# Optimization experiments

Hardware: AMD Instinct MI355X
Metric: run time of the kernel (lower is better)

The kernel has to match this reference:

```python
import jax, jax.numpy as jnp
import numpy as np

EPS = 1e-8  # torch CosineSimilarity eps


def _l2_normalize(x):
    n = jnp.sqrt(jnp.sum(x * x, axis=-1, keepdims=True))
    return x / jnp.maximum(n, EPS)


def setup_inputs() -> dict:
    key = jax.random.key(0)
    k1, k2, k3 = jax.random.split(key, 3)
    B, D, K = 4096, 1024, 256
    datapoints = jax.random.normal(k1, (B, D), dtype=jnp.float32)
    centroid = jax.random.normal(k2, (K, D), dtype=jnp.float32)
    batch_cos_sim = jax.random.normal(k3, (B, B), dtype=jnp.float32)
    return {"datapoints": datapoints, "centroid": centroid, "batch_cos_sim": batch_cos_sim}


def reference(datapoints, centroid, batch_cos_sim):
    # --- _clustering: cosine similarity datapoints[B,D] vs centroid[K,D] (temp=1) ---
    dn = _l2_normalize(datapoints)                       # [B, D]
    cn = _l2_normalize(centroid)                         # [K, D]
    intra_cos_sim = jnp.einsum('bd,kd->bk', dn, cn)      # [B, K]
    dp_index = jnp.argmax(intra_cos_sim, axis=-1)        # [B]

    # --- _intra_class_adjacency: one-hot matmul, zero diagonal ---
    onehot = jax.nn.one_hot(dp_index, centroid.shape[0], dtype=jnp.float32)  # [B, K]
    dp_cluster = jnp.einsum('bk,ck->bc', onehot, onehot)                      # [B, B]
    B = datapoints.shape[0]
    dp_cluster = dp_cluster * (1.0 - jnp.eye(B, dtype=dp_cluster.dtype))
    index_dp = onehot.T.astype(jnp.int32)                # [K, B]

    # --- gather centroid each datapoint belongs to ---
    dp_centroid = centroid[dp_index]                     # [B, D]

    # --- provide_hard_negative: top-2, take 2nd-best centroid ---
    top_vals, top_idx = jax.lax.top_k(intra_cos_sim, 2)  # [B, 2]
    hard_neg_index = top_idx[:, 1]                       # [B]
    hard_negative = centroid[hard_neg_index]             # [B, D]

    return (intra_cos_sim, dp_index, dp_cluster, index_dp, dp_centroid,
            hard_negative, hard_neg_index, top_vals[:, 1])
```

## Files before the change

### kernel.cpp

```cpp
#include <hip/hip_runtime.h>
#include <hip/hip_bf16.h>
#include <math.h>

#define B_N 4096
#define D_N 1024
#define K_N 256
#define NSTEP 32

typedef __attribute__((ext_vector_type(8))) short bf16x8;
typedef __attribute__((ext_vector_type(8))) unsigned short u16x8;
typedef __attribute__((ext_vector_type(4))) float f32x4;

static constexpr float K_EPS = 1e-8f;

static __device__ __forceinline__ unsigned short f32_to_bf16_rne(float f) {
    unsigned x = __builtin_bit_cast(unsigned, f);
    unsigned r = (x + 0x7FFFu + ((x >> 16) & 1u)) >> 16;
    return (unsigned short)r;
}
static __device__ __forceinline__ float bf16_bits_to_f32(unsigned short h) {
    unsigned x = ((unsigned)h) << 16;
    return __builtin_bit_cast(float, x);
}
static __device__ __forceinline__ void cvt8(
    float e0, float e1, float e2, float e3,
    float e4, float e5, float e6, float e7, u16x8& hv, u16x8& lv)
{
    ushort h0=f32_to_bf16_rne(e0), h1=f32_to_bf16_rne(e1),
           h2=f32_to_bf16_rne(e2), h3=f32_to_bf16_rne(e3),
           h4=f32_to_bf16_rne(e4), h5=f32_to_bf16_rne(e5),
           h6=f32_to_bf16_rne(e6), h7=f32_to_bf16_rne(e7);
    hv = (u16x8){h0,h1,h2,h3,h4,h5,h6,h7};
    lv = (u16x8){f32_to_bf16_rne(e0 - bf16_bits_to_f32(h0)),
                 f32_to_bf16_rne(e1 - bf16_bits_to_f32(h1)),
                 f32_to_bf16_rne(e2 - bf16_bits_to_f32(h2)),
                 f32_to_bf16_rne(e3 - bf16_bits_to_f32(h3)),
                 f32_to_bf16_rne(e4 - bf16_bits_to_f32(h4)),
                 f32_to_bf16_rne(e5 - bf16_bits_to_f32(h5)),
                 f32_to_bf16_rne(e6 - bf16_bits_to_f32(h6)),
                 f32_to_bf16_rne(e7 - bf16_bits_to_f32(h7))};
}

__global__ __launch_bounds__(256) void kcent_kernel(
    const float* __restrict__ cent,
    ushort* __restrict__ phi, ushort* __restrict__ plo)
{
    int n   = blockIdx.x;
    int tid = threadIdx.x;
    float4 v = reinterpret_cast<const float4*>(cent + (size_t)n * D_N)[tid];
    float s = v.x * v.x + v.y * v.y + v.z * v.z + v.w * v.w;
    #pragma unroll
    for (int o = 32; o > 0; o >>= 1) s += __shfl_down(s, o);
    __shared__ float red[4];
    __shared__ float s_inv;
    if ((tid & 63) == 0) red[tid >> 6] = s;
    __syncthreads();
    if (tid == 0) {
        float t = red[0] + red[1] + red[2] + red[3];
        s_inv = 1.0f / fmaxf(sqrtf(t), K_EPS);
    }
    __syncthreads();
    float inv = s_inv;
    float e[4] = {v.x * inv, v.y * inv, v.z * inv, v.w * inv};
    ushort h4[4], l4[4];
    #pragma unroll
    for (int j = 0; j < 4; ++j) {
        ushort h = f32_to_bf16_rne(e[j]);
        float lo = e[j] - bf16_bits_to_f32(h);
        h4[j] = h;
        l4[j] = f32_to_bf16_rne(lo);
    }
    int nt = n >> 4, lr = n & 15;
    int k8 = tid >> 1, half = tid & 1;
    int t  = k8 >> 2, lg = k8 & 3;
    size_t chunk = (size_t)(nt * 32 + t) * 64 + lg * 16 + lr;
    *reinterpret_cast<ushort4*>(phi + chunk * 8 + half * 4) =
        make_ushort4(h4[0], h4[1], h4[2], h4[3]);
    *reinterpret_cast<ushort4*>(plo + chunk * 8 + half * 4) =
        make_ushort4(l4[0], l4[1], l4[2], l4[3]);
}

__global__ __launch_bounds__(1024) void kmain_kernel(
    const float* __restrict__ dp, const float* __restrict__ cent,
    const ushort* __restrict__ phi, const ushort* __restrict__ plo,
    float* __restrict__ out_sims, float* __restrict__ out_dpidx,
    float* __restrict__ out_hnidx, float* __restrict__ out_top1,
    float* __restrict__ out_dpcent, float* __restrict__ out_hneg,
    int* __restrict__ ws_dpidx)
{
    __shared__ ushort AhL[16 * 1024];
    __shared__ ushort AlL[16 * 1024];
    __shared__ float  simsL[16 * 256];
    int tid  = threadIdx.x;
    int lane = tid & 63;
    int w    = tid >> 6;
    int lr   = lane & 15;
    int lg   = lane >> 4;
    int brow = blockIdx.x * 16;

    const ushort* bh = phi + (size_t)w * 32 * 512 + (size_t)lane * 8;
    const ushort* bl = plo + (size_t)w * 32 * 512 + (size_t)lane * 8;

    #define LBF(t, H, L)                                                  \
        H = *reinterpret_cast<const bf16x8*>(bh + (size_t)(t) * 512);     \
        L = *reinterpret_cast<const bf16x8*>(bl + (size_t)(t) * 512);

    bf16x8 h0,l0,h1,l1,h2,l2,h3,l3,h4,l4,h5,l5,h6,l6,h7,l7;
    LBF(0,h0,l0) LBF(1,h1,l1) LBF(2,h2,l2) LBF(3,h3,l3)
    LBF(4,h4,l4) LBF(5,h5,l5) LBF(6,h6,l6) LBF(7,h7,l7)

    {
        const float4* r4 = reinterpret_cast<const float4*>(
            dp + (size_t)(brow + w) * D_N);
        float4 a0 = r4[lane*4+0], a1 = r4[lane*4+1],
               a2 = r4[lane*4+2], a3 = r4[lane*4+3];
        float s = a0.x*a0.x + a0.y*a0.y + a0.z*a0.z + a0.w*a0.w
                + a1.x*a1.x + a1.y*a1.y + a1.z*a1.z + a1.w*a1.w
                + a2.x*a2.x + a2.y*a2.y + a2.z*a2.z + a2.w*a2.w
                + a3.x*a3.x + a3.y*a3.y + a3.z*a3.z + a3.w*a3.w;
        #pragma unroll
        for (int o = 1; o < 64; o <<= 1) s += __shfl_xor(s, o);
        float inv = 1.0f / fmaxf(sqrtf(s), K_EPS);
        u16x8 hv, lv;
        cvt8(a0.x*inv, a0.y*inv, a0.z*inv, a0.w*inv,
             a1.x*inv, a1.y*inv, a1.z*inv, a1.w*inv, hv, lv);
        int slot = (lane*2 + 0) ^ (w & 7);
        *reinterpret_cast<u16x8*>(&AhL[w*1024 + slot*8]) = hv;
        *reinterpret_cast<u16x8*>(&AlL[w*1024 + slot*8]) = lv;
        cvt8(a2.x*inv, a2.y*inv, a2.z*inv, a2.w*inv,
             a3.x*inv, a3.y*inv, a3.z*inv, a3.w*inv, hv, lv);
        slot = (lane*2 + 1) ^ (w & 7);
        *reinterpret_cast<u16x8*>(&AhL[w*1024 + slot*8]) = hv;
        *reinterpret_cast<u16x8*>(&AlL[w*1024 + slot*8]) = lv;
    }
    __syncthreads();

    f32x4 acc = {};
    const char* AhC = (const char*)AhL;
    const char* AlC = (const char*)AlL;
    auto step = [&](int t, bf16x8 hb, bf16x8 lb) {
        unsigned ca = (unsigned)((4*t + lg) ^ (lr & 7));
        unsigned ao = (unsigned)lr * 2048u + ca * 16u;
        bf16x8 ah = *reinterpret_cast<const bf16x8*>(AhC + ao);
        bf16x8 al = *reinterpret_cast<const bf16x8*>(AlC + ao);
        acc = __builtin_amdgcn_mfma_f32_16x16x32_bf16(ah, hb, acc, 0, 0, 0);
        acc = __builtin_amdgcn_mfma_f32_16x16x32_bf16(ah, lb, acc, 0, 0, 0);
        acc = __builtin_amdgcn_mfma_f32_16x16x32_bf16(al, hb, acc, 0, 0, 0);
    };
    #pragma unroll 1
    for (int t = 0; t < NSTEP; t += 8) {
        step(t + 0, h0, l0); if (t +  8 < NSTEP) { LBF(t +  8, h0, l0) }
        step(t + 1, h1, l1); if (t +  9 < NSTEP) { LBF(t +  9, h1, l1) }
        step(t + 2, h2, l2); if (t + 10 < NSTEP) { LBF(t + 10, h2, l2) }
        step(t + 3, h3, l3); if (t + 11 < NSTEP) { LBF(t + 11, h3, l3) }
        step(t + 4, h4, l4); if (t + 12 < NSTEP) { LBF(t + 12, h4, l4) }
        step(t + 5, h5, l5); if (t + 13 < NSTEP) { LBF(t + 13, h5, l5) }
        step(t + 6, h6, l6); if (t + 14 < NSTEP) { LBF(t + 14, h6, l6) }
        step(t + 7, h7, l7); if (t + 15 < NSTEP) { LBF(t + 15, h7, l7) }
    }
    #undef LBF

    #pragma unroll
    for (int r = 0; r < 4; ++r)
        simsL[(lg*4 + r) * K_N + w*16 + lr] = acc[r];
    __syncthreads();

    {
        float4 c = *reinterpret_cast<const float4*>(&simsL[w * K_N + lane * 4]);
        int row = brow + w;
        *reinterpret_cast<float4*>(&out_sims[(size_t)row * K_N + lane * 4]) = c;
        float v1b = c.x; int i1 = lane * 4;
        float v2b = -INFINITY; int i2 = 0;
        {
            float vals[3] = {c.y, c.z, c.w};
            #pragma unroll
            for (int j = 0; j < 3; ++j) {
                float val = vals[j]; int idx = lane * 4 + j + 1;
                if (val > v1b) { v2b = v1b; i2 = i1; v1b = val; i1 = idx; }
                else if (val > v2b) { v2b = val; i2 = idx; }
            }
        }
        #pragma unroll
        for (int o = 1; o < 64; o <<= 1) {
            float ov1 = __shfl_xor(v1b, o);
            float ov2 = __shfl_xor(v2b, o);
            int   oi1 = __shfl_xor(i1, o);
            int   oi2 = __shfl_xor(i2, o);
            if (ov1 > v1b || (ov1 == v1b && oi1 < i1)) {
                float nv2; int ni2;
                if (v1b > ov2 || (v1b == ov2 && i1 < oi2)) { nv2 = v1b; ni2 = i1; }
                else { nv2 = ov2; ni2 = oi2; }
                v1b = ov1; i1 = oi1; v2b = nv2; i2 = ni2;
            } else if (ov1 > v2b || (ov1 == v2b && oi1 < i2)) {
                v2b = ov1; i2 = oi1;
            }
        }
        const float4* cent4 = reinterpret_cast<const float4*>(cent);
        #pragma unroll
        for (int q = 0; q < 4; ++q) {
            float4 g1 = cent4[(size_t)i1 * 256 + q * 64 + lane];
            float4 g2 = cent4[(size_t)i2 * 256 + q * 64 + lane];
            reinterpret_cast<float4*>(out_dpcent + (size_t)row * D_N)[q*64 + lane] = g1;
            reinterpret_cast<float4*>(out_hneg   + (size_t)row * D_N)[q*64 + lane] = g2;
        }
        if (lane == 0) {
            out_dpidx[row] = (float)i1;
            out_hnidx[row] = (float)i2;
            out_top1[row]  = v2b;
            ws_dpidx[row]  = i1;
        }
    }
}

__global__ __launch_bounds__(256) void kclust_kernel(
    const int* __restrict__ dpidx,
    float* __restrict__ out_cluster, float* __restrict__ out_indexdp)
{
    int bid  = blockIdx.x;
    int tid  = threadIdx.x;
    int base = bid * 4;
    const int4* dpi4 = reinterpret_cast<const int4*>(dpidx);

    int4 ixq[4];
    #pragma unroll
    for (int q = 0; q < 4; ++q) ixq[q] = dpi4[q * 256 + tid];

    if (base < B_N) {
        int4 me4 = dpi4[bid];
        int mes[4] = {me4.x, me4.y, me4.z, me4.w};
        #pragma unroll
        for (int r = 0; r < 4; ++r) {
            int gr = base + r;
            int me = mes[r];
            float* dst = out_cluster + (size_t)gr * B_N;
            #pragma unroll
            for (int q = 0; q < 4; ++q) {
                int j = q * 1024 + tid * 4;
                float4 v;
                v.x = (ixq[q].x == me && (j + 0) != gr) ? 1.0f : 0.0f;
                v.y = (ixq[q].y == me && (j + 1) != gr) ? 1.0f : 0.0f;
                v.z = (ixq[q].z == me && (j + 2) != gr) ? 1.0f : 0.0f;
                v.w = (ixq[q].w == me && (j + 3) != gr) ? 1.0f : 0.0f;
                *reinterpret_cast<float4*>(dst + j) = v;
            }
        }
    } else {
        #pragma unroll
        for (int r = 0; r < 4; ++r) {
            int k = base + r - B_N;
            float* dst = out_indexdp + (size_t)k * B_N;
            #pragma unroll
            for (int q = 0; q < 4; ++q) {
                int j = q * 1024 + tid * 4;
                float4 v;
                v.x = (ixq[q].x == k) ? 1.0f : 0.0f;
                v.y = (ixq[q].y == k) ? 1.0f : 0.0f;
                v.z = (ixq[q].z == k) ? 1.0f : 0.0f;
                v.w = (ixq[q].w == k) ? 1.0f : 0.0f;
                *reinterpret_cast<float4*>(dst + j) = v;
            }
        }
    }
}

extern "C" void kernel_launch(void* const* d_in, const int* in_sizes, int n_in,
                              void* d_out, int out_size, void* d_ws, size_t ws_size,
                              hipStream_t stream)
{
    const float* dp   = (const float*)d_in[0];
    const float* cent = (const float*)d_in[1];
    float* out = (float*)d_out;

    float* o_sims   = out;
    float* o_dpidx  = out + 1048576;
    float* o_clust  = out + 1052672;
    float* o_idxdp  = out + 17829888;
    float* o_dpcent = out + 18878464;
    float* o_hneg   = out + 23072768;
    float* o_hnidx  = out + 27267072;
    float* o_top1   = out + 27271168;

    char* ws = (char*)d_ws;
    ushort* phi  = (ushort*)ws;
    ushort* plo  = (ushort*)(ws + (512u << 10));
    int*    widx = (int*)(ws + (1u << 20));

    hipLaunchKernelGGL(kcent_kernel, dim3(K_N), dim3(256), 0, stream,
                       cent, phi, plo);
    hipLaunchKernelGGL(kmain_kernel, dim3(B_N / 16), dim3(1024), 0, stream,
                       dp, cent, phi, plo,
                       o_sims, o_dpidx, o_hnidx, o_top1,
                       o_dpcent, o_hneg, widx);
    hipLaunchKernelGGL(kclust_kernel, dim3((B_N + K_N) / 4), dim3(256), 0, stream,
                       widx, o_clust, o_idxdp);
}
```

Baseline: 43.81 us.

## Move centroid gathers from the matmul kernel into the write kernel

The main similarity kernel no longer gathers centroid rows into the dp_centroid and hard_negative outputs. It now stores the hard-negative index to workspace. A merged write kernel gives one block per datapoint to copy both gathered rows, followed by the cluster-adjacency blocks. This moves 32 MB of gather writes out of the low-occupancy 256-block main kernel into a wide, fully parallel kernel, at the cost of a longer final kernel and one extra index buffer.

```diff
diff --git a/kernel.cpp b/kernel.cpp
--- a/kernel.cpp
+++ b/kernel.cpp
@@ -81,12 +81,11 @@
 }
 
 __global__ __launch_bounds__(1024) void kmain_kernel(
-    const float* __restrict__ dp, const float* __restrict__ cent,
+    const float* __restrict__ dp,
     const ushort* __restrict__ phi, const ushort* __restrict__ plo,
     float* __restrict__ out_sims, float* __restrict__ out_dpidx,
     float* __restrict__ out_hnidx, float* __restrict__ out_top1,
-    float* __restrict__ out_dpcent, float* __restrict__ out_hneg,
-    int* __restrict__ ws_dpidx)
+    int* __restrict__ ws_dpidx, int* __restrict__ ws_hnidx)
 {
     __shared__ ushort AhL[16 * 1024];
     __shared__ ushort AlL[16 * 1024];
@@ -195,38 +194,42 @@
                 v2b = ov1; i2 = oi1;
             }
         }
-        const float4* cent4 = reinterpret_cast<const float4*>(cent);
-        #pragma unroll
-        for (int q = 0; q < 4; ++q) {
-            float4 g1 = cent4[(size_t)i1 * 256 + q * 64 + lane];
-            float4 g2 = cent4[(size_t)i2 * 256 + q * 64 + lane];
-            reinterpret_cast<float4*>(out_dpcent + (size_t)row * D_N)[q*64 + lane] = g1;
-            reinterpret_cast<float4*>(out_hneg   + (size_t)row * D_N)[q*64 + lane] = g2;
-        }
         if (lane == 0) {
             out_dpidx[row] = (float)i1;
             out_hnidx[row] = (float)i2;
             out_top1[row]  = v2b;
             ws_dpidx[row]  = i1;
-        }
-    }
-}
-
-__global__ __launch_bounds__(256) void kclust_kernel(
-    const int* __restrict__ dpidx,
+            ws_hnidx[row]  = i2;
+        }
+    }
+}
+
+__global__ __launch_bounds__(256) void kwrite_kernel(
+    const float* __restrict__ cent,
+    const int* __restrict__ dpidx, const int* __restrict__ hnidx,
+    float* __restrict__ out_dpcent, float* __restrict__ out_hneg,
     float* __restrict__ out_cluster, float* __restrict__ out_indexdp)
 {
-    int bid  = blockIdx.x;
-    int tid  = threadIdx.x;
-    int base = bid * 4;
+    int bid = blockIdx.x;
+    int tid = threadIdx.x;
+    if (bid < B_N) {
+        int b = bid;
+        int i1 = dpidx[b], i2 = hnidx[b];
+        float4 v1 = reinterpret_cast<const float4*>(cent + (size_t)i1 * D_N)[tid];
+        float4 v2 = reinterpret_cast<const float4*>(cent + (size_t)i2 * D_N)[tid];
+        reinterpret_cast<float4*>(out_dpcent + (size_t)b * D_N)[tid] = v1;
+        reinterpret_cast<float4*>(out_hneg   + (size_t)b * D_N)[tid] = v2;
+        return;
+    }
+    int cb   = bid - B_N;
+    int base = cb * 4;
     const int4* dpi4 = reinterpret_cast<const int4*>(dpidx);
-
     int4 ixq[4];
     #pragma unroll
     for (int q = 0; q < 4; ++q) ixq[q] = dpi4[q * 256 + tid];
 
     if (base < B_N) {
-        int4 me4 = dpi4[bid];
+        int4 me4 = dpi4[cb];
         int mes[4] = {me4.x, me4.y, me4.z, me4.w};
         #pragma unroll
         for (int r = 0; r < 4; ++r) {
@@ -284,13 +287,14 @@
     ushort* phi  = (ushort*)ws;
     ushort* plo  = (ushort*)(ws + (512u << 10));
     int*    widx = (int*)(ws + (1u << 20));
+    int*    whn  = (int*)(ws + (1u << 20) + 16384);
 
     hipLaunchKernelGGL(kcent_kernel, dim3(K_N), dim3(256), 0, stream,
                        cent, phi, plo);
     hipLaunchKernelGGL(kmain_kernel, dim3(B_N / 16), dim3(1024), 0, stream,
-                       dp, cent, phi, plo,
-                       o_sims, o_dpidx, o_hnidx, o_top1,
-                       o_dpcent, o_hneg, widx);
-    hipLaunchKernelGGL(kclust_kernel, dim3((B_N + K_N) / 4), dim3(256), 0, stream,
-                       widx, o_clust, o_idxdp);
-}
+                       dp, phi, plo,
+                       o_sims, o_dpidx, o_hnidx, o_top1, widx, whn);
+    hipLaunchKernelGGL(kwrite_kernel, dim3(B_N + 1088), dim3(256), 0, stream,
+                       cent, widx, whn,
+                       o_dpcent, o_hneg, o_clust, o_idxdp);
+}
```

Result: no change. 44.58 us (+1.8%).
